# Performance work log

Measured on AMD Instinct MI355X. Metric: run time of the kernel, lower is better.

Reference implementation:

```python
import jax, jax.numpy as jnp
import numpy as np

E, N, D_IN, HID, TD, H = 800000, 50000, 64, 32, 32, 4
HO = H * HID
VOCAB = 1000000


def time_encode(t, dim):
    # t: [E,1] -> [E,dim], interleaved sin/cos harmonic encoding
    div_term = jnp.exp(jnp.arange(0, dim, 2, dtype=jnp.float32) * (-jnp.log(10000.0) / dim))
    ang = t * div_term  # [E, dim//2]
    return jnp.stack([jnp.sin(ang), jnp.cos(ang)], axis=-1).reshape(t.shape[0], dim)


def tgat_conv(x, src, dst, t_feat, wq, bq, wk, bk, wv, bv, wt, bt, num_nodes):
    # x: [N, Fin]; t_feat: [E, TD]
    q = (x @ wq + bq).reshape(-1, H, HID)
    k = (x @ wk + bk).reshape(-1, H, HID)
    v = (x @ wv + bv).reshape(-1, H, HID)
    te = (t_feat @ wt + bt).reshape(-1, H, HID)
    q_i = q[dst]                      # [E,H,HID] gather at target
    k_j = k[src] + te                 # [E,H,HID] gather at source + time enc
    alpha = jnp.sum(q_i * k_j, axis=-1) / jnp.sqrt(jnp.float32(HID))  # [E,H]
    # segment softmax over edges grouped by destination node
    m = jax.ops.segment_max(alpha, dst, num_segments=num_nodes)        # [N,H]
    ex = jnp.exp(alpha - m[dst])
    s = jax.ops.segment_sum(ex, dst, num_segments=num_nodes)           # [N,H]
    a = ex / (s[dst] + 1e-16)                                          # [E,H]
    msg = v[src] * a[:, :, None]                                       # [E,H,HID]
    out = jax.ops.segment_sum(msg, dst, num_segments=num_nodes)        # [N,H,HID]
    return out.reshape(num_nodes, HO)


def setup_inputs() -> dict:
    key = jax.random.key(0)
    ks = jax.random.split(key, 24)

    def lin_w(k, fi, fo):
        return jax.random.normal(k, (fi, fo), dtype=jnp.float32) / jnp.sqrt(jnp.float32(fi))

    inp = {
        'edge_index': jax.random.randint(ks[0], (2, E), 0, N),
        'edge_attr': jax.random.uniform(ks[1], (E, 2), dtype=jnp.float32),
        'num_nodes': N,
        'emb': jax.random.normal(ks[2], (VOCAB, D_IN), dtype=jnp.float32) * 0.1,
        'wq1': lin_w(ks[3], D_IN, HO), 'bq1': jnp.zeros((HO,), jnp.float32),
        'wk1': lin_w(ks[4], D_IN, HO), 'bk1': jnp.zeros((HO,), jnp.float32),
        'wv1': lin_w(ks[5], D_IN, HO), 'bv1': jnp.zeros((HO,), jnp.float32),
        'wt1': lin_w(ks[6], TD, HO), 'bt1': jnp.zeros((HO,), jnp.float32),
        'wq2': lin_w(ks[7], HO, HO), 'bq2': jnp.zeros((HO,), jnp.float32),
        'wk2': lin_w(ks[8], HO, HO), 'bk2': jnp.zeros((HO,), jnp.float32),
        'wv2': lin_w(ks[9], HO, HO), 'bv2': jnp.zeros((HO,), jnp.float32),
        'wt2': lin_w(ks[10], TD, HO), 'bt2': jnp.zeros((HO,), jnp.float32),
        'wc': lin_w(ks[11], HO, 1), 'bc': jnp.zeros((1,), jnp.float32),
    }
    return inp


def reference(edge_index, edge_attr, num_nodes, emb,
              wq1, bq1, wk1, bk1, wv1, bv1, wt1, bt1,
              wq2, bq2, wk2, bk2, wv2, bv2, wt2, bt2,
              wc, bc):
    src, dst = edge_index[0], edge_index[1]
    x = emb[:num_nodes]                                   # node_emb(arange(N))
    raw_time = edge_attr[:, 1:2]                          # [E,1]
    t_feat = time_encode(raw_time, TD)                    # [E,TD]
    x = jax.nn.relu(tgat_conv(x, src, dst, t_feat, wq1, bq1, wk1, bk1, wv1, bv1, wt1, bt1, num_nodes))
    x = jax.nn.relu(tgat_conv(x, src, dst, t_feat, wq2, bq2, wk2, bk2, wv2, bv2, wt2, bt2, num_nodes))
    edge_emb = x[src] + x[dst]                            # [E,HO]
    return (edge_emb @ wc + bc).squeeze(-1)               # [E]
```

## Files before the change

### kernel.cpp

```cpp
#include <hip/hip_runtime.h>
#include <hip/hip_bf16.h>

#define NNODES 50000
#define HOUT   128
#define NHEAD  4
#define HID    32
#define TDIM   32

typedef _Float16 h8 __attribute__((ext_vector_type(8)));
typedef _Float16 h4 __attribute__((ext_vector_type(4)));
typedef float    f4 __attribute__((ext_vector_type(4)));

__constant__ float DIVT_REV[16] = {
    0.15915494309189535f,   0.08950140093327467f,   0.050329212595f,        0.028302204f,
    0.015915494309189535f,  0.008950140093327467f,  0.0050329212595f,       0.0028302204f,
    0.0015915494309189535f, 0.0008950140093327467f, 0.00050329212595f,      0.00028302204f,
    0.00015915494309189535f,0.00008950140093327467f,0.000050329212595f,     0.000028302204f
};

__global__ __launch_bounds__(128) void prep_layer_kernel(
    const float* __restrict__ wq, const float* __restrict__ wk,
    const float* __restrict__ wv, const float* __restrict__ wt,
    const float* __restrict__ bq,
    _Float16* __restrict__ hi, _Float16* __restrict__ lo,
    float* __restrict__ bqt, int din)
{
    const int y = blockIdx.y, col = blockIdx.x, k = threadIdx.x;
    float w;
    if (y < 3) {
        const float* W = (y == 0) ? wq : (y == 1) ? wk : wv;
        w = W[(size_t)k * HOUT + col];
    } else {
        const int h = col >> 5, t = col & 31;
        const float* wqr = wq + (size_t)k * HOUT + h * 32;
        const float* wtr = wt + (size_t)t * HOUT + h * 32;
        float s = 0.f;
        #pragma unroll
        for (int d2 = 0; d2 < 32; d2++) s += wqr[d2] * wtr[d2];
        w = s;
        if (k == 0) {
            float sb = 0.f;
            #pragma unroll
            for (int d2 = 0; d2 < 32; d2++) sb += bq[h * 32 + d2] * wtr[d2];
            bqt[col] = sb;
        }
    }
    const _Float16 h16 = (_Float16)w;
    const size_t idx = ((size_t)y * HOUT + col) * din + k;
    hi[idx] = h16;
    lo[idx] = (_Float16)(w - (float)h16);
}

#define GPITCH 72

__global__ __launch_bounds__(256) void gemm_qkv_mfma_kernel(
    const float* __restrict__ X, int din, int n,
    const _Float16* __restrict__ Whi, const _Float16* __restrict__ Wlo,
    const float* __restrict__ B0, const float* __restrict__ B1,
    const float* __restrict__ B2, const float* __restrict__ B3,
    float* __restrict__ q, _Float16* __restrict__ kv, float* __restrict__ qwt)
{
    const int y = blockIdx.y;
    const float* B = (y == 0) ? B0 : (y == 1) ? B1 : (y == 2) ? B2 : B3;
    const _Float16* Wy_hi = Whi + (size_t)y * HOUT * din;
    const _Float16* Wy_lo = Wlo + (size_t)y * HOUT * din;

    __shared__ _Float16 Xh[64 * GPITCH];
    __shared__ _Float16 Xl[64 * GPITCH];
    __shared__ _Float16 Bh[128 * GPITCH];
    __shared__ _Float16 Bl[128 * GPITCH];

    const int tid  = threadIdx.x;
    const int row0 = blockIdx.x * 64;
    const int wv   = tid >> 6;
    const int lane = tid & 63;
    const int lm   = lane & 15;
    const int g    = lane >> 4;

    f4 acc[8];
    #pragma unroll
    for (int ct = 0; ct < 8; ct++) acc[ct] = (f4){0.f, 0.f, 0.f, 0.f};

    float bias[8];
    #pragma unroll
    for (int ct = 0; ct < 8; ct++) bias[ct] = B[ct * 16 + lm];

    const int ktiles = din >> 6;
    for (int kt = 0; kt < ktiles; kt++) {
        {
            const int lrow = tid >> 2;
            const int k0   = (tid & 3) << 4;
            const int grow = row0 + lrow;
            const float* src = X + (size_t)grow * din + kt * 64 + k0;
            #pragma unroll
            for (int i = 0; i < 4; i++) {
                float4 v = (grow < n) ? ((const float4*)src)[i]
                                      : make_float4(0.f, 0.f, 0.f, 0.f);
                h4 hi, lo;
                hi[0] = (_Float16)v.x; hi[1] = (_Float16)v.y;
                hi[2] = (_Float16)v.z; hi[3] = (_Float16)v.w;
                lo[0] = (_Float16)(v.x - (float)hi[0]);
                lo[1] = (_Float16)(v.y - (float)hi[1]);
                lo[2] = (_Float16)(v.z - (float)hi[2]);
                lo[3] = (_Float16)(v.w - (float)hi[3]);
                *(h4*)&Xh[lrow * GPITCH + k0 + 4 * i] = hi;
                *(h4*)&Xl[lrow * GPITCH + k0 + 4 * i] = lo;
            }
        }
        {
            const int col = tid >> 1;
            const int kk0 = (tid & 1) << 5;
            const _Float16* sh = Wy_hi + (size_t)col * din + kt * 64 + kk0;
            const _Float16* sl = Wy_lo + (size_t)col * din + kt * 64 + kk0;
            #pragma unroll
            for (int i = 0; i < 4; i++) {
                *(h8*)&Bh[col * GPITCH + kk0 + 8 * i] = ((const h8*)sh)[i];
                *(h8*)&Bl[col * GPITCH + kk0 + 8 * i] = ((const h8*)sl)[i];
            }
        }
        __syncthreads();

        #pragma unroll
        for (int kc = 0; kc < 2; kc++) {
            const int kb = kc * 32 + g * 8;
            const h8 ah = *(const h8*)&Xh[(wv * 16 + lm) * GPITCH + kb];
            const h8 al = *(const h8*)&Xl[(wv * 16 + lm) * GPITCH + kb];
            #pragma unroll
            for (int ct = 0; ct < 8; ct++) {
                const h8 bh = *(const h8*)&Bh[(ct * 16 + lm) * GPITCH + kb];
                const h8 bl = *(const h8*)&Bl[(ct * 16 + lm) * GPITCH + kb];
                acc[ct] = __builtin_amdgcn_mfma_f32_16x16x32_f16(ah, bh, acc[ct], 0, 0, 0);
                acc[ct] = __builtin_amdgcn_mfma_f32_16x16x32_f16(al, bh, acc[ct], 0, 0, 0);
                acc[ct] = __builtin_amdgcn_mfma_f32_16x16x32_f16(ah, bl, acc[ct], 0, 0, 0);
            }
        }
        __syncthreads();
    }

    #pragma unroll
    for (int ct = 0; ct < 8; ct++) {
        const int col = ct * 16 + lm;
        #pragma unroll
        for (int r = 0; r < 4; r++) {
            const int grow = row0 + wv * 16 + g * 4 + r;
            if (grow >= n) continue;
            const float o = acc[ct][r] + bias[ct];
            if (y == 0)      q[(size_t)grow * HOUT + col] = o;
            else if (y == 3) qwt[(size_t)grow * HOUT + col] = o;
            else             kv[(size_t)grow * 256 + ((y == 1) ? 0 : 128) + col] = (_Float16)o;
        }
    }
}

__global__ __launch_bounds__(256) void hist_kernel(
    const int* __restrict__ ei, int* __restrict__ cnt, int E)
{
    const int e = blockIdx.x * 256 + threadIdx.x;
    if (e >= E) return;
    atomicAdd(&cnt[ei[E + e]], 1);
}

__global__ __launch_bounds__(256) void scan_sum_kernel(
    const int* __restrict__ cnt, int* __restrict__ bsum, int n4)
{
    const int i = blockIdx.x * 256 + threadIdx.x;
    int s = 0;
    if (i < n4) { int4 c = ((const int4*)cnt)[i]; s = c.x + c.y + c.z + c.w; }
    #pragma unroll
    for (int d = 1; d < 64; d <<= 1) s += __shfl_xor(s, d);
    __shared__ int wsum[4];
    if ((threadIdx.x & 63) == 0) wsum[threadIdx.x >> 6] = s;
    __syncthreads();
    if (threadIdx.x == 0) bsum[blockIdx.x] = wsum[0] + wsum[1] + wsum[2] + wsum[3];
}

__global__ __launch_bounds__(256) void scan_write_kernel(
    const int* __restrict__ cnt, const int* __restrict__ bsum,
    int* __restrict__ off, int n4, int nb, int E)
{
    __shared__ int bpre_s;
    __shared__ int wsum[4];
    const int lane = threadIdx.x & 63;
    if (threadIdx.x < 64) {
        int v = (lane < nb) ? bsum[lane] : 0;
        int incl = v;
        #pragma unroll
        for (int d = 1; d < 64; d <<= 1) {
            int u = __shfl_up(incl, d);
            if (lane >= d) incl += u;
        }
        const int pre = (blockIdx.x == 0) ? 0 : __shfl(incl, blockIdx.x - 1);
        if (threadIdx.x == 0) bpre_s = pre;
    }

    const int i = blockIdx.x * 256 + threadIdx.x;
    int4 c = make_int4(0, 0, 0, 0);
    if (i < n4) c = ((const int4*)cnt)[i];
    const int s = c.x + c.y + c.z + c.w;
    int incl = s;
    #pragma unroll
    for (int d = 1; d < 64; d <<= 1) {
        int u = __shfl_up(incl, d);
        if (lane >= d) incl += u;
    }
    const int wv = threadIdx.x >> 6;
    __syncthreads();
    if (lane == 63) wsum[wv] = incl;
    __syncthreads();
    int base = bpre_s;
    for (int w = 0; w < wv; w++) base += wsum[w];
    const int excl = base + incl - s;
    if (i < n4)
        ((int4*)off)[i] = make_int4(excl, excl + c.x, excl + c.x + c.y,
                                    excl + c.x + c.y + c.z);
    if (blockIdx.x == 0 && threadIdx.x == 0) off[NNODES] = E;
}

__global__ __launch_bounds__(256) void scatter_kernel(
    const int* __restrict__ ei, const float* __restrict__ ea,
    const int* __restrict__ off, int* __restrict__ cur,
    int2* __restrict__ recs, int E)
{
    const int e = blockIdx.x * 256 + threadIdx.x;
    if (e >= E) return;
    const int dn = ei[E + e];
    const int pos = off[dn] + atomicAdd(&cur[dn], 1);
    recs[pos] = make_int2(ei[e], __float_as_int(ea[2 * e + 1]));
}

__global__ __launch_bounds__(256) void node_attn_kernel(
    const int* __restrict__ off, const int2* __restrict__ recs,
    const float* __restrict__ q, const _Float16* __restrict__ kv,
    const float* __restrict__ qwt, const float* __restrict__ bt,
    float* __restrict__ x, const float* __restrict__ wc,
    float* __restrict__ p, int n)
{
    const int wid = (blockIdx.x * 256 + threadIdx.x) >> 6;
    if (wid >= n) return;
    const int lane = threadIdx.x & 63;
    const int slot = lane >> 4;
    const int sub  = lane & 15;
    const int c0   = sub * 8;
    const int dn   = wid;
    const int i0   = (sub & 3) * 4;

    const float4* qv = (const float4*)(q   + (size_t)dn * HOUT + c0);
    const float4* wv = (const float4*)(qwt + (size_t)dn * HOUT + c0);
    const float4 q0 = qv[0], q1 = qv[1];
    const float4 w0 = wv[0], w1 = wv[1];

    const float4 bt0 = ((const float4*)(bt + c0))[0];
    const float4 bt1 = ((const float4*)(bt + c0))[1];
    float qb = q0.x * bt0.x + q0.y * bt0.y + q0.z * bt0.z + q0.w * bt0.w +
               q1.x * bt1.x + q1.y * bt1.y + q1.z * bt1.z + q1.w * bt1.w;
    qb += __shfl_xor(qb, 1);
    qb += __shfl_xor(qb, 2);

    const int beg = off[dn];
    const int end = off[dn + 1];

    float acc[8] = {0.f, 0.f, 0.f, 0.f, 0.f, 0.f, 0.f, 0.f};
    float den = 0.f;

    int i = beg + slot;
    int2 rec0 = make_int2(0, 0), rec1 = make_int2(0, 0);
    h8 kk = {0, 0, 0, 0, 0, 0, 0, 0};
    h8 vv = {0, 0, 0, 0, 0, 0, 0, 0};
    if (i < end)     rec0 = recs[i];
    if (i + 4 < end) rec1 = recs[i + 4];
    if (i < end) {
        const _Float16* kp = kv + (size_t)rec0.x * 256 + c0;
        kk = *(const h8*)kp;
        vv = *(const h8*)(kp + 128);
    }

    while (i < end) {
        int2 rec2 = make_int2(0, 0);
        if (i + 8 < end) rec2 = recs[i + 8];
        h8 kkn = kk, vvn = vv;
        if (i + 4 < end) {
            const _Float16* kp = kv + (size_t)rec1.x * 256 + c0;
            kkn = *(const h8*)kp;
            vvn = *(const h8*)(kp + 128);
        }

        const float rt = __int_as_float(rec0.y);
        float tf[8];
        #pragma unroll
        for (int jj = 0; jj < 4; jj++) {
            const float rev = rt * DIVT_REV[i0 + jj];
            tf[2 * jj]     = __builtin_amdgcn_sinf(rev);
            tf[2 * jj + 1] = __builtin_amdgcn_cosf(rev);
        }

        float partial =
            q0.x * (float)kk[0] + q0.y * (float)kk[1] +
            q0.z * (float)kk[2] + q0.w * (float)kk[3] +
            q1.x * (float)kk[4] + q1.y * (float)kk[5] +
            q1.z * (float)kk[6] + q1.w * (float)kk[7] +
            w0.x * tf[0] + w0.y * tf[1] + w0.z * tf[2] + w0.w * tf[3] +
            w1.x * tf[4] + w1.y * tf[5] + w1.z * tf[6] + w1.w * tf[7];
        if ((sub & 3) == 0) partial += qb;

        partial += __shfl_xor(partial, 1);
        partial += __shfl_xor(partial, 2);

        const float ex = __expf(partial * 0.17677669529663687f);
        den += ex;
        #pragma unroll
        for (int j = 0; j < 8; j++) acc[j] += ex * (float)vv[j];

        i += 4;
        rec0 = rec1; rec1 = rec2; kk = kkn; vv = vvn;
    }

    #pragma unroll
    for (int j = 0; j < 8; j++) {
        acc[j] += __shfl_xor(acc[j], 16);
        acc[j] += __shfl_xor(acc[j], 32);
    }
    den += __shfl_xor(den, 16);
    den += __shfl_xor(den, 32);

    if (lane < 16) {
        const float inv = 1.f / (den + 1e-16f);
        float o[8];
        #pragma unroll
        for (int j = 0; j < 8; j++) o[j] = fmaxf(acc[j] * inv, 0.f);
        if (p == nullptr) {
            float* xo = x + (size_t)dn * HOUT + c0;
            *(float4*)xo       = make_float4(o[0], o[1], o[2], o[3]);
            *((float4*)xo + 1) = make_float4(o[4], o[5], o[6], o[7]);
        } else {
            const float4 wc0 = ((const float4*)(wc + c0))[0];
            const float4 wc1 = ((const float4*)(wc + c0))[1];
            float pp = o[0] * wc0.x + o[1] * wc0.y + o[2] * wc0.z + o[3] * wc0.w +
                       o[4] * wc1.x + o[5] * wc1.y + o[6] * wc1.z + o[7] * wc1.w;
            pp += __shfl_xor(pp, 1);
            pp += __shfl_xor(pp, 2);
            pp += __shfl_xor(pp, 4);
            pp += __shfl_xor(pp, 8);
            if (sub == 0) p[dn] = pp;
        }
    }
}

__global__ __launch_bounds__(256) void edge_out_kernel(
    const int* __restrict__ ei, const float* __restrict__ p,
    const float* __restrict__ bc, float* __restrict__ out, int E)
{
    const int e = blockIdx.x * 256 + threadIdx.x;
    if (e >= E) return;
    out[e] = p[ei[e]] + p[ei[E + e]] + bc[0];
}

extern "C" void kernel_launch(void* const* d_in, const int* in_sizes, int n_in,
                              void* d_out, int out_size, void* d_ws, size_t ws_size,
                              hipStream_t stream)
{
    const int E = in_sizes[0] / 2;
    const int N = NNODES;

    const int*   ei  = (const int*)d_in[0];
    const float* ea  = (const float*)d_in[1];
    const float* emb = (const float*)d_in[3];
    const float *wq1 = (const float*)d_in[4],  *bq1 = (const float*)d_in[5];
    const float *wk1 = (const float*)d_in[6],  *bk1 = (const float*)d_in[7];
    const float *wv1 = (const float*)d_in[8],  *bv1 = (const float*)d_in[9];
    const float *wt1 = (const float*)d_in[10], *bt1 = (const float*)d_in[11];
    const float *wq2 = (const float*)d_in[12], *bq2 = (const float*)d_in[13];
    const float *wk2 = (const float*)d_in[14], *bk2 = (const float*)d_in[15];
    const float *wv2 = (const float*)d_in[16], *bv2 = (const float*)d_in[17];
    const float *wt2 = (const float*)d_in[18], *bt2 = (const float*)d_in[19];
    const float *wc  = (const float*)d_in[20], *bc  = (const float*)d_in[21];
    float* out = (float*)d_out;

    float* ws = (float*)d_ws;
    const size_t NF = (size_t)N * HOUT;
    float*     q    = ws;
    float*     qwt  = ws + NF;
    float*     xbuf = ws + 2 * NF;
    _Float16*  kv   = (_Float16*)(ws + 3 * NF);
    int2*      recs = (int2*)(ws + 4 * NF);
    float*     bqt1 = (float*)(recs + E);
    float*     bqt2 = bqt1 + HOUT;
    _Float16*  whi1 = (_Float16*)(bqt2 + HOUT);
    _Float16*  wlo1 = whi1 + 4 * HOUT * 64;
    _Float16*  whi2 = wlo1 + 4 * HOUT * 64;
    _Float16*  wlo2 = whi2 + 4 * HOUT * 128;
    int*       cnt  = (int*)(wlo2 + 4 * HOUT * 128);
    int*       off  = cnt + N;
    int*       cur  = off + N + 1;
    float*     p    = (float*)(cur + N);
    int*       bsum = (int*)(p + N);

    const dim3 ggemm((N + 63) / 64, 4);
    const int  eblk  = (E + 255) / 256;
    const int  nblk  = (N + 3) / 4;
    const int  n4    = N / 4;
    const int  sblk  = (n4 + 255) / 256;

    prep_layer_kernel<<<dim3(HOUT, 4), 64, 0, stream>>>(
        wq1, wk1, wv1, wt1, bq1, whi1, wlo1, bqt1, 64);
    prep_layer_kernel<<<dim3(HOUT, 4), 128, 0, stream>>>(
        wq2, wk2, wv2, wt2, bq2, whi2, wlo2, bqt2, 128);

    hipMemsetAsync(cnt, 0, (size_t)N * sizeof(int), stream);
    hipMemsetAsync(cur, 0, (size_t)N * sizeof(int), stream);
    hist_kernel<<<eblk, 256, 0, stream>>>(ei, cnt, E);
    scan_sum_kernel<<<sblk, 256, 0, stream>>>(cnt, bsum, n4);
    scan_write_kernel<<<sblk, 256, 0, stream>>>(cnt, bsum, off, n4, sblk, E);
    scatter_kernel<<<eblk, 256, 0, stream>>>(ei, ea, off, cur, recs, E);

    gemm_qkv_mfma_kernel<<<ggemm, 256, 0, stream>>>(emb, 64, N,
        whi1, wlo1, bq1, bk1, bv1, bqt1, q, kv, qwt);
    node_attn_kernel<<<nblk, 256, 0, stream>>>(off, recs, q, kv, qwt, bt1,
                                               xbuf, nullptr, nullptr, N);

    gemm_qkv_mfma_kernel<<<ggemm, 256, 0, stream>>>(xbuf, 128, N,
        whi2, wlo2, bq2, bk2, bv2, bqt2, q, kv, qwt);
    node_attn_kernel<<<nblk, 256, 0, stream>>>(off, recs, q, kv, qwt, bt2,
                                               nullptr, wc, p, N);

    edge_out_kernel<<<(E + 255) / 256, 256, 0, stream>>>(ei, p, bc, out, E);
}
```

Measured before the change: 648.0 us.

## Merge prep launches, record ranks in histogram, single-block scan, vectorize edge kernels

Both layers' weight-prep launches become one grid, and that grid also zeroes the count array, so the memsets go away. The histogram saves each edge's atomic rank as a ushort, which lets the scatter drop its second atomic pass and the cur array. The two-kernel scan becomes one single-block scan with a 1024-thread loop. The edge kernels now process 2-4 edges per thread with vector loads. These changes cut launch count and atomic traffic, but the single-block scan is serial across tiles and the ranks assume in-degree stays below 65536.

Result: faster. 626.0 us (median of 2 runs) (-3.4%).

```diff
diff --git a/kernel.cpp b/kernel.cpp
--- a/kernel.cpp
+++ b/kernel.cpp
@@ -18,14 +18,35 @@
     0.00015915494309189535f,0.00008950140093327467f,0.000050329212595f,     0.000028302204f
 };
 
-__global__ __launch_bounds__(128) void prep_layer_kernel(
-    const float* __restrict__ wq, const float* __restrict__ wk,
-    const float* __restrict__ wv, const float* __restrict__ wt,
-    const float* __restrict__ bq,
-    _Float16* __restrict__ hi, _Float16* __restrict__ lo,
-    float* __restrict__ bqt, int din)
-{
+__global__ __launch_bounds__(128) void prep_kernel(
+    const float* __restrict__ wq1, const float* __restrict__ wk1,
+    const float* __restrict__ wv1, const float* __restrict__ wt1,
+    const float* __restrict__ bq1,
+    const float* __restrict__ wq2, const float* __restrict__ wk2,
+    const float* __restrict__ wv2, const float* __restrict__ wt2,
+    const float* __restrict__ bq2,
+    _Float16* __restrict__ hi1, _Float16* __restrict__ lo1, float* __restrict__ bqt1,
+    _Float16* __restrict__ hi2, _Float16* __restrict__ lo2, float* __restrict__ bqt2,
+    int* __restrict__ cnt)
+{
+    const int flat = ((blockIdx.z * 4 + blockIdx.y) * HOUT + blockIdx.x) * 128
+                     + threadIdx.x;
+    if (flat < NNODES) cnt[flat] = 0;
+
+    const int layer = blockIdx.z;
+    const int din   = layer ? 128 : 64;
     const int y = blockIdx.y, col = blockIdx.x, k = threadIdx.x;
+    if (k >= din) return;
+
+    const float* wq = layer ? wq2 : wq1;
+    const float* wk = layer ? wk2 : wk1;
+    const float* wv = layer ? wv2 : wv1;
+    const float* wt = layer ? wt2 : wt1;
+    const float* bq = layer ? bq2 : bq1;
+    _Float16* hi = layer ? hi2 : hi1;
+    _Float16* lo = layer ? lo2 : lo1;
+    float*   bqt = layer ? bqt2 : bqt1;
+
     float w;
     if (y < 3) {
         const float* W = (y == 0) ? wq : (y == 1) ? wk : wv;
@@ -153,79 +174,74 @@
 }
 
 __global__ __launch_bounds__(256) void hist_kernel(
-    const int* __restrict__ ei, int* __restrict__ cnt, int E)
-{
-    const int e = blockIdx.x * 256 + threadIdx.x;
-    if (e >= E) return;
-    atomicAdd(&cnt[ei[E + e]], 1);
-}
-
-__global__ __launch_bounds__(256) void scan_sum_kernel(
-    const int* __restrict__ cnt, int* __restrict__ bsum, int n4)
-{
-    const int i = blockIdx.x * 256 + threadIdx.x;
-    int s = 0;
-    if (i < n4) { int4 c = ((const int4*)cnt)[i]; s = c.x + c.y + c.z + c.w; }
-    #pragma unroll
-    for (int d = 1; d < 64; d <<= 1) s += __shfl_xor(s, d);
-    __shared__ int wsum[4];
-    if ((threadIdx.x & 63) == 0) wsum[threadIdx.x >> 6] = s;
-    __syncthreads();
-    if (threadIdx.x == 0) bsum[blockIdx.x] = wsum[0] + wsum[1] + wsum[2] + wsum[3];
-}
-
-__global__ __launch_bounds__(256) void scan_write_kernel(
-    const int* __restrict__ cnt, const int* __restrict__ bsum,
-    int* __restrict__ off, int n4, int nb, int E)
-{
-    __shared__ int bpre_s;
-    __shared__ int wsum[4];
-    const int lane = threadIdx.x & 63;
-    if (threadIdx.x < 64) {
-        int v = (lane < nb) ? bsum[lane] : 0;
-        int incl = v;
+    const int* __restrict__ ei, int* __restrict__ cnt,
+    unsigned short* __restrict__ rank, int E)
+{
+    const int e4 = (blockIdx.x * 256 + threadIdx.x) * 4;
+    if (e4 >= E) return;
+    const int4 d = *(const int4*)&ei[E + e4];
+    rank[e4 + 0] = (unsigned short)atomicAdd(&cnt[d.x], 1);
+    rank[e4 + 1] = (unsigned short)atomicAdd(&cnt[d.y], 1);
+    rank[e4 + 2] = (unsigned short)atomicAdd(&cnt[d.z], 1);
+    rank[e4 + 3] = (unsigned short)atomicAdd(&cnt[d.w], 1);
+}
+
+__global__ __launch_bounds__(1024) void scan_kernel(
+    const int* __restrict__ cnt, int* __restrict__ off, int E)
+{
+    __shared__ int wsums[16];
+    __shared__ int wexcl[16];
+    __shared__ int tile_tot;
+    const int tid = threadIdx.x, lane = tid & 63, wv = tid >> 6;
+    const int n4 = NNODES / 4;
+    int carry = 0;
+    for (int base4 = 0; base4 < n4; base4 += 1024) {
+        const int ti = base4 + tid;
+        int4 c = make_int4(0, 0, 0, 0);
+        if (ti < n4) c = ((const int4*)cnt)[ti];
+        const int s = c.x + c.y + c.z + c.w;
+        int incl = s;
         #pragma unroll
         for (int d = 1; d < 64; d <<= 1) {
             int u = __shfl_up(incl, d);
             if (lane >= d) incl += u;
         }
-        const int pre = (blockIdx.x == 0) ? 0 : __shfl(incl, blockIdx.x - 1);
-        if (threadIdx.x == 0) bpre_s = pre;
-    }
-
-    const int i = blockIdx.x * 256 + threadIdx.x;
-    int4 c = make_int4(0, 0, 0, 0);
-    if (i < n4) c = ((const int4*)cnt)[i];
-    const int s = c.x + c.y + c.z + c.w;
-    int incl = s;
-    #pragma unroll
-    for (int d = 1; d < 64; d <<= 1) {
-        int u = __shfl_up(incl, d);
-        if (lane >= d) incl += u;
-    }
-    const int wv = threadIdx.x >> 6;
-    __syncthreads();
-    if (lane == 63) wsum[wv] = incl;
-    __syncthreads();
-    int base = bpre_s;
-    for (int w = 0; w < wv; w++) base += wsum[w];
-    const int excl = base + incl - s;
-    if (i < n4)
-        ((int4*)off)[i] = make_int4(excl, excl + c.x, excl + c.x + c.y,
-                                    excl + c.x + c.y + c.z);
-    if (blockIdx.x == 0 && threadIdx.x == 0) off[NNODES] = E;
+        if (lane == 63) wsums[wv] = incl;
+        __syncthreads();
+        if (tid < 16) {
+            const int w = wsums[tid];
+            int iw = w;
+            #pragma unroll
+            for (int d = 1; d < 16; d <<= 1) {
+                int u = __shfl_up(iw, d);
+                if (tid >= d) iw += u;
+            }
+            wexcl[tid] = iw - w;
+            if (tid == 15) tile_tot = iw;
+        }
+        __syncthreads();
+        const int excl = carry + wexcl[wv] + (incl - s);
+        if (ti < n4)
+            ((int4*)off)[ti] = make_int4(excl, excl + c.x, excl + c.x + c.y,
+                                         excl + c.x + c.y + c.z);
+        carry += tile_tot;
+        __syncthreads();
+    }
+    if (tid == 0) off[NNODES] = E;
 }
 
 __global__ __launch_bounds__(256) void scatter_kernel(
     const int* __restrict__ ei, const float* __restrict__ ea,
-    const int* __restrict__ off, int* __restrict__ cur,
+    const int* __restrict__ off, const unsigned short* __restrict__ rank,
     int2* __restrict__ recs, int E)
 {
-    const int e = blockIdx.x * 256 + threadIdx.x;
-    if (e >= E) return;
-    const int dn = ei[E + e];
-    const int pos = off[dn] + atomicAdd(&cur[dn], 1);
-    recs[pos] = make_int2(ei[e], __float_as_int(ea[2 * e + 1]));
+    const int e2 = (blockIdx.x * 256 + threadIdx.x) * 2;
+    if (e2 >= E) return;
+    const int2 s = *(const int2*)&ei[e2];
+    const int2 d = *(const int2*)&ei[E + e2];
+    const float4 t4 = *(const float4*)&ea[2 * e2];
+    recs[off[d.x] + rank[e2]]     = make_int2(s.x, __float_as_int(t4.y));
+    recs[off[d.y] + rank[e2 + 1]] = make_int2(s.y, __float_as_int(t4.w));
 }
 
 __global__ __launch_bounds__(256) void node_attn_kernel(
@@ -349,9 +365,15 @@
     const int* __restrict__ ei, const float* __restrict__ p,
     const float* __restrict__ bc, float* __restrict__ out, int E)
 {
-    const int e = blockIdx.x * 256 + threadIdx.x;
-    if (e >= E) return;
-    out[e] = p[ei[e]] + p[ei[E + e]] + bc[0];
+    const int e4 = (blockIdx.x * 256 + threadIdx.x) * 4;
+    if (e4 >= E) return;
+    const int4 s = *(const int4*)&ei[e4];
+    const int4 d = *(const int4*)&ei[E + e4];
+    const float b = bc[0];
+    *(float4*)&out[e4] = make_float4(p[s.x] + p[d.x] + b,
+                                     p[s.y] + p[d.y] + b,
+                                     p[s.z] + p[d.z] + b,
+                                     p[s.w] + p[d.w] + b);
 }
 
 extern "C" void kernel_launch(void* const* d_in, const int* in_sizes, int n_in,
@@ -390,27 +412,22 @@
     _Float16*  wlo2 = whi2 + 4 * HOUT * 128;
     int*       cnt  = (int*)(wlo2 + 4 * HOUT * 128);
     int*       off  = cnt + N;
-    int*       cur  = off + N + 1;
-    float*     p    = (float*)(cur + N);
-    int*       bsum = (int*)(p + N);
+    float*     p    = (float*)(off + N + 1);
+    unsigned short* rank = (unsigned short*)(p + N);
 
     const dim3 ggemm((N + 63) / 64, 4);
-    const int  eblk  = (E + 255) / 256;
     const int  nblk  = (N + 3) / 4;
-    const int  n4    = N / 4;
-    const int  sblk  = (n4 + 255) / 256;
-
-    prep_layer_kernel<<<dim3(HOUT, 4), 64, 0, stream>>>(
-        wq1, wk1, wv1, wt1, bq1, whi1, wlo1, bqt1, 64);
-    prep_layer_kernel<<<dim3(HOUT, 4), 128, 0, stream>>>(
-        wq2, wk2, wv2, wt2, bq2, whi2, wlo2, bqt2, 128);
-
-    hipMemsetAsync(cnt, 0, (size_t)N * sizeof(int), stream);
-    hipMemsetAsync(cur, 0, (size_t)N * sizeof(int), stream);
-    hist_kernel<<<eblk, 256, 0, stream>>>(ei, cnt, E);
-    scan_sum_kernel<<<sblk, 256, 0, stream>>>(cnt, bsum, n4);
-    scan_write_kernel<<<sblk, 256, 0, stream>>>(cnt, bsum, off, n4, sblk, E);
-    scatter_kernel<<<eblk, 256, 0, stream>>>(ei, ea, off, cur, recs, E);
+    const int  hblk  = (E + 1023) / 1024;
+    const int  scblk = (E + 511) / 512;
+    const int  eoblk = (E + 1023) / 1024;
+
+    prep_kernel<<<dim3(HOUT, 4, 2), 128, 0, stream>>>(
+        wq1, wk1, wv1, wt1, bq1, wq2, wk2, wv2, wt2, bq2,
+        whi1, wlo1, bqt1, whi2, wlo2, bqt2, cnt);
+
+    hist_kernel<<<hblk, 256, 0, stream>>>(ei, cnt, rank, E);
+    scan_kernel<<<1, 1024, 0, stream>>>(cnt, off, E);
+    scatter_kernel<<<scblk, 256, 0, stream>>>(ei, ea, off, rank, recs, E);
 
     gemm_qkv_mfma_kernel<<<ggemm, 256, 0, stream>>>(emb, 64, N,
         whi1, wlo1, bq1, bk1, bv1, bqt1, q, kv, qwt);
@@ -422,5 +439,5 @@
     node_attn_kernel<<<nblk, 256, 0, stream>>>(off, recs, q, kv, qwt, bt2,
                                                nullptr, wc, p, N);
 
-    edge_out_kernel<<<(E + 255) / 256, 256, 0, stream>>>(ei, p, bc, out, E);
-}
+    edge_out_kernel<<<eoblk, 256, 0, stream>>>(ei, p, bc, out, E);
+}
```
